# Optimization experiments

Hardware: AMD Instinct MI355X
Metric: run time of the kernel (lower is better)

Reference implementation:

```python
import jax, jax.numpy as jnp
import numpy as np

N = 10000
D1, D2, D3, N_INPUT = 20, 256, 128, 500


def setup_inputs() -> dict:
    key = jax.random.key(0)
    k1, k2, k3, k4, k5 = jax.random.split(key, 5)
    z_igae = jax.random.normal(k1, (N, D1), dtype=jnp.float32)
    # row-stochastic-ish dense (normalized) adjacency stand-in
    adj = jax.random.uniform(k2, (N, N), dtype=jnp.float32) / N
    w3 = jax.random.normal(k3, (D1, D2), dtype=jnp.float32) * 0.1
    w4 = jax.random.normal(k4, (D2, D3), dtype=jnp.float32) * 0.1
    w5 = jax.random.normal(k5, (D3, N_INPUT), dtype=jnp.float32) * 0.1
    return {"z_igae": z_igae, "adj": adj, "w3": w3, "w4": w4, "w5": w5}


def reference(z_igae, adj, w3, w4, w5):
    # GNNLayer: spmm(adj, x @ W), tanh activation when active=True
    z = jnp.tanh(adj @ (z_igae @ w3))        # [N, D2]
    z = jnp.tanh(adj @ (z @ w4))             # [N, D3]
    z_hat = adj @ (z @ w5)                   # [N, n_input], active=False
    z_hat_adj = jax.nn.sigmoid(z_hat @ z_hat.T)  # [N, N] dense reconstruction
    return (z_hat, z_hat_adj)
```

## Files before the change

kernel.cpp:

```cpp
#include <hip/hip_runtime.h>
#include <cstddef>
#include <cstdint>


typedef __attribute__((ext_vector_type(8))) short bf16x8;
typedef __attribute__((ext_vector_type(4))) float f32x4;

#define NROWS 10000
#define MP 10048
#define MP2 10112

__device__ inline unsigned short f2bf(float f) {
  union { float f; unsigned int u; } a; a.f = f;
  unsigned int u = a.u;
  u += 0x7fffu + ((u >> 16) & 1u);
  return (unsigned short)(u >> 16);
}

__device__ inline void gl_lds16(const void* g, void* l) {
  __builtin_amdgcn_global_load_lds(
      (const __attribute__((address_space(1))) void*)g,
      (__attribute__((address_space(3))) void*)l, 16, 0, 0);
}

__global__ __launch_bounds__(256)
void gemm1_fused(const float* __restrict__ adj, const short* __restrict__ zt,
                 short* __restrict__ adjb, float* __restrict__ P,
                 int kChunks, int S) {
  __shared__ short As[64 * 64];
  __shared__ short Bs[32 * 64];
  const int tid  = threadIdx.x;
  const int wave = tid >> 6;
  const int lane = tid & 63;
  const int row0 = blockIdx.y * 64;
  const int s    = blockIdx.z;
  const int t0 = (int)((long long)s * kChunks / S);
  const int t1 = (int)((long long)(s + 1) * kChunks / S);

  f32x4 acc[2];
#pragma unroll
  for (int i = 0; i < 2; ++i) acc[i] = (f32x4){0.f, 0.f, 0.f, 0.f};

  const int lr = lane >> 3;
  const int lk = ((lane & 7) ^ lr) * 8;
  const int fr = lane & 15, fq = lane >> 4, sw = lane & 7;

  const int ar  = tid >> 2;
  const int acq = tid & 3;
  const int gr  = row0 + ar;
  const bool rv = gr < NROWS;

  for (int t = t0; t < t1; ++t) {
    const int k0 = t * 64;
    __syncthreads();
    gl_lds16(zt + (size_t)(8 * wave + lr) * MP + k0 + lk, (void*)(Bs + wave * 512));
    const int gc = k0 + acq * 16;
    float4 f[4];
#pragma unroll
    for (int j = 0; j < 4; ++j) {
      int c = gc + 4 * j;
      f[j] = (rv && c < NROWS) ? *(const float4*)(adj + (size_t)gr * NROWS + c)
                               : make_float4(0.f, 0.f, 0.f, 0.f);
    }
    unsigned short h[16] __attribute__((aligned(16)));
#pragma unroll
    for (int j = 0; j < 4; ++j) {
      h[4 * j + 0] = f2bf(f[j].x); h[4 * j + 1] = f2bf(f[j].y);
      h[4 * j + 2] = f2bf(f[j].z); h[4 * j + 3] = f2bf(f[j].w);
    }
    *(uint4*)(adjb + (size_t)gr * MP + gc)     = *(const uint4*)&h[0];
    *(uint4*)(adjb + (size_t)gr * MP + gc + 8) = *(const uint4*)&h[8];
    *(bf16x8*)&As[ar * 64 + ((acq * 2 + 0) ^ (ar & 7)) * 8] = *(const bf16x8*)&h[0];
    *(bf16x8*)&As[ar * 64 + ((acq * 2 + 1) ^ (ar & 7)) * 8] = *(const bf16x8*)&h[8];
    __syncthreads();
#pragma unroll
    for (int ks = 0; ks < 2; ++ks) {
      const int go = ((ks * 4 + fq) ^ sw) * 8;
      bf16x8 af = *(const bf16x8*)&As[(wave * 16 + fr) * 64 + go];
#pragma unroll
      for (int nt = 0; nt < 2; ++nt) {
        bf16x8 bfr = *(const bf16x8*)&Bs[(nt * 16 + fr) * 64 + go];
        acc[nt] = __builtin_amdgcn_mfma_f32_16x16x32_bf16(af, bfr, acc[nt], 0, 0, 0);
      }
    }
  }
  float* Cs = P + (size_t)s * MP * 32;
  const int rbase = row0 + wave * 16 + (lane >> 4) * 4;
  const int cbase = lane & 15;
#pragma unroll
  for (int nt = 0; nt < 2; ++nt) {
    const int cc = cbase + nt * 16;
#pragma unroll
    for (int r = 0; r < 4; ++r)
      Cs[(size_t)(rbase + r) * 32 + cc] = acc[nt][r];
  }
}

template <int NT>
__global__ __launch_bounds__(256)
void gemm_bf16(const short* __restrict__ A, int lda,
               const short* __restrict__ Bt, int ldb,
               float* __restrict__ C, long long cSplitStride, int ldc,
               int kChunks, int S) {
  __shared__ short As[2][64 * 64];
  __shared__ short Bs[2][NT * 64];
  const int tid  = threadIdx.x;
  const int wave = tid >> 6;
  const int lane = tid & 63;
  const int row0 = blockIdx.y * 64;
  const int col0 = blockIdx.x * NT;
  const int s    = blockIdx.z;
  const int t0 = (int)((long long)s * kChunks / S);
  const int t1 = (int)((long long)(s + 1) * kChunks / S);

  f32x4 acc[NT / 16];
#pragma unroll
  for (int i = 0; i < NT / 16; ++i) acc[i] = (f32x4){0.f, 0.f, 0.f, 0.f};

  const int lr = lane >> 3;
  const int lk = ((lane & 7) ^ lr) * 8;
  const int fr = lane & 15, fq = lane >> 4, sw = lane & 7;

  auto stage = [&](int b, int t) {
    const int k0 = t * 64;
#pragma unroll
    for (int i = 0; i < 2; ++i) {
      int c = wave + 4 * i;
      gl_lds16(A + (size_t)(row0 + 8 * c + lr) * lda + k0 + lk,
               (void*)(&As[b][c * 512]));
    }
#pragma unroll
    for (int i = 0; i < NT / 32; ++i) {
      int c = wave + 4 * i;
      gl_lds16(Bt + (size_t)(col0 + 8 * c + lr) * ldb + k0 + lk,
               (void*)(&Bs[b][c * 512]));
    }
  };

  stage(0, t0);
  for (int t = t0; t < t1; ++t) {
    const int b = (t - t0) & 1;
    __syncthreads();
    if (t + 1 < t1) stage(b ^ 1, t + 1);
#pragma unroll
    for (int ks = 0; ks < 2; ++ks) {
      const int go = ((ks * 4 + fq) ^ sw) * 8;
      bf16x8 af = *(const bf16x8*)&As[b][(wave * 16 + fr) * 64 + go];
#pragma unroll
      for (int nt = 0; nt < NT / 16; ++nt) {
        bf16x8 bfr = *(const bf16x8*)&Bs[b][(nt * 16 + fr) * 64 + go];
        acc[nt] = __builtin_amdgcn_mfma_f32_16x16x32_bf16(af, bfr, acc[nt], 0, 0, 0);
      }
    }
  }

  float* Cs = C + (long long)s * cSplitStride;
  const int rbase = row0 + wave * 16 + (lane >> 4) * 4;
  const int cbase = col0 + (lane & 15);
#pragma unroll
  for (int nt = 0; nt < NT / 16; ++nt) {
    const int cc = cbase + nt * 16;
#pragma unroll
    for (int r = 0; r < 4; ++r)
      Cs[(size_t)(rbase + r) * ldc + cc] = acc[nt][r];
  }
}

__global__ __launch_bounds__(256)
void gemm_recon(const short* __restrict__ A, const short* __restrict__ Bt,
                float* __restrict__ C) {
  __shared__ short As[128 * 64];
  __shared__ short Bs[128 * 64];
  const int tid  = threadIdx.x;
  const int wave = tid >> 6;
  const int lane = tid & 63;
  const int row0 = blockIdx.y * 128;
  const int col0 = blockIdx.x * 128;

  f32x4 acc[2][8];
#pragma unroll
  for (int i = 0; i < 2; ++i)
#pragma unroll
    for (int j = 0; j < 8; ++j) acc[i][j] = (f32x4){0.f, 0.f, 0.f, 0.f};

  const int lr = lane >> 3;
  const int lk = ((lane & 7) ^ lr) * 8;
  const int fr = lane & 15, fq = lane >> 4, sw = lane & 7;

  for (int t = 0; t < 2; ++t) {
    const int k0 = t * 64;
    __syncthreads();
#pragma unroll
    for (int i = 0; i < 4; ++i) {
      int c = wave + 4 * i;
      gl_lds16(A + (size_t)(row0 + 8 * c + lr) * 128 + k0 + lk, (void*)(As + c * 512));
      gl_lds16(Bt + (size_t)(col0 + 8 * c + lr) * 128 + k0 + lk, (void*)(Bs + c * 512));
    }
    __syncthreads();
#pragma unroll
    for (int ks = 0; ks < 2; ++ks) {
      const int go = ((ks * 4 + fq) ^ sw) * 8;
      bf16x8 a0 = *(const bf16x8*)&As[(wave * 32 + fr) * 64 + go];
      bf16x8 a1 = *(const bf16x8*)&As[(wave * 32 + 16 + fr) * 64 + go];
#pragma unroll
      for (int nt = 0; nt < 8; ++nt) {
        bf16x8 bfr = *(const bf16x8*)&Bs[(nt * 16 + fr) * 64 + go];
        acc[0][nt] = __builtin_amdgcn_mfma_f32_16x16x32_bf16(a0, bfr, acc[0][nt], 0, 0, 0);
        acc[1][nt] = __builtin_amdgcn_mfma_f32_16x16x32_bf16(a1, bfr, acc[1][nt], 0, 0, 0);
      }
    }
  }

  const int q = lane >> 4;
#pragma unroll
  for (int mf = 0; mf < 2; ++mf) {
    const int rb = row0 + wave * 32 + mf * 16 + q * 4;
#pragma unroll
    for (int nt = 0; nt < 8; ++nt) {
      const int cc = col0 + nt * 16 + (lane & 15);
      if (cc >= NROWS) continue;
#pragma unroll
      for (int r = 0; r < 4; ++r) {
        const int rr = rb + r;
        if (rr < NROWS) {
          float v = acc[mf][nt][r];
          v = 1.0f / (1.0f + __expf(-v));
          C[(size_t)rr * NROWS + cc] = v;
        }
      }
    }
  }
}

#define TK 16
#define TM 64
#define TN 64

template <int ACT, bool OBF16>
__global__ __launch_bounds__(256)
void gemm_nn_f32(const float* __restrict__ A, int lda,
                 const float* __restrict__ B, int ldb,
                 void* __restrict__ Cp, int ldc, int M, int N, int K) {
  __shared__ float Asm[TK][TM + 4];
  __shared__ float Bsm[TK][TN + 4];
  const int tid = threadIdx.x;
  const int tx = tid & 15, ty = tid >> 4;
  const int row0 = blockIdx.y * TM, col0 = blockIdx.x * TN;
  const int a_m = tid >> 2, a_k = (tid & 3) << 2;
  const int b_k = tid >> 4, b_n = (tid & 15) << 2;
  float acc[4][4] = {};
  const int ntile = (K + TK - 1) / TK;

  auto ld_a = [&](int k0) {
    float4 v = make_float4(0.f, 0.f, 0.f, 0.f);
    int r = row0 + a_m, k = k0 + a_k;
    if (r < M && k < K) v = *(const float4*)(A + (size_t)r * lda + k);
    return v;
  };
  auto ld_b = [&](int k0) {
    float4 v = make_float4(0.f, 0.f, 0.f, 0.f);
    int k = k0 + b_k, c = col0 + b_n;
    if (k < K && c + 3 < N) v = *(const float4*)(B + (size_t)k * ldb + c);
    return v;
  };

  float4 pa = ld_a(0), pb = ld_b(0);
  for (int t = 0; t < ntile; ++t) {
    __syncthreads();
    Asm[a_k + 0][a_m] = pa.x; Asm[a_k + 1][a_m] = pa.y;
    Asm[a_k + 2][a_m] = pa.z; Asm[a_k + 3][a_m] = pa.w;
    *(float4*)&Bsm[b_k][b_n] = pb;
    __syncthreads();
    if (t + 1 < ntile) { pa = ld_a((t + 1) * TK); pb = ld_b((t + 1) * TK); }
#pragma unroll
    for (int kk = 0; kk < TK; ++kk) {
      float4 a = *(const float4*)&Asm[kk][ty << 2];
      float4 b = *(const float4*)&Bsm[kk][tx << 2];
      float av[4] = {a.x, a.y, a.z, a.w};
      float bv[4] = {b.x, b.y, b.z, b.w};
#pragma unroll
      for (int i = 0; i < 4; ++i)
#pragma unroll
        for (int j = 0; j < 4; ++j) acc[i][j] += av[i] * bv[j];
    }
  }
#pragma unroll
  for (int i = 0; i < 4; ++i) {
    int r = row0 + (ty << 2) + i;
    if (r >= M) continue;
#pragma unroll
    for (int j = 0; j < 4; ++j) {
      int c = col0 + (tx << 2) + j;
      if (c >= N) continue;
      float v = acc[i][j];
      if (ACT == 1) v = tanhf(v);
      if (OBF16) ((unsigned short*)Cp)[(size_t)r * ldc + c] = f2bf(v);
      else       ((float*)Cp)[(size_t)r * ldc + c] = v;
    }
  }
}

template <int ACT>
__global__ __launch_bounds__(256)
void gemm_nt_f32(const float* __restrict__ A, int lda,
                 const float* __restrict__ B, int ldb,
                 float* __restrict__ C, int ldc, int M, int N, int K) {
  __shared__ float Asm[TK][TM + 4];
  __shared__ float Bsm[TK][TN + 4];
  const int tid = threadIdx.x;
  const int tx = tid & 15, ty = tid >> 4;
  const int row0 = blockIdx.y * TM, col0 = blockIdx.x * TN;
  const int a_m = tid >> 2, a_k = (tid & 3) << 2;
  const int b_n = tid >> 2, b_k = (tid & 3) << 2;
  float acc[4][4] = {};
  const int ntile = (K + TK - 1) / TK;

  auto ld_a = [&](int k0) {
    float4 v = make_float4(0.f, 0.f, 0.f, 0.f);
    int r = row0 + a_m, k = k0 + a_k;
    if (r < M && k + 3 < K) v = *(const float4*)(A + (size_t)r * lda + k);
    return v;
  };
  auto ld_b = [&](int k0) {
    float4 v = make_float4(0.f, 0.f, 0.f, 0.f);
    int c = col0 + b_n, k = k0 + b_k;
    if (c < N && k + 3 < K) v = *(const float4*)(B + (size_t)c * ldb + k);
    return v;
  };

  float4 pa = ld_a(0), pb = ld_b(0);
  for (int t = 0; t < ntile; ++t) {
    __syncthreads();
    Asm[a_k + 0][a_m] = pa.x; Asm[a_k + 1][a_m] = pa.y;
    Asm[a_k + 2][a_m] = pa.z; Asm[a_k + 3][a_m] = pa.w;
    Bsm[b_k + 0][b_n] = pb.x; Bsm[b_k + 1][b_n] = pb.y;
    Bsm[b_k + 2][b_n] = pb.z; Bsm[b_k + 3][b_n] = pb.w;
    __syncthreads();
    if (t + 1 < ntile) { pa = ld_a((t + 1) * TK); pb = ld_b((t + 1) * TK); }
#pragma unroll
    for (int kk = 0; kk < TK; ++kk) {
      float4 a = *(const float4*)&Asm[kk][ty << 2];
      float4 b = *(const float4*)&Bsm[kk][tx << 2];
      float av[4] = {a.x, a.y, a.z, a.w};
      float bv[4] = {b.x, b.y, b.z, b.w};
#pragma unroll
      for (int i = 0; i < 4; ++i)
#pragma unroll
        for (int j = 0; j < 4; ++j) acc[i][j] += av[i] * bv[j];
    }
  }
#pragma unroll
  for (int i = 0; i < 4; ++i) {
    int r = row0 + (ty << 2) + i;
    if (r >= M) continue;
#pragma unroll
    for (int j = 0; j < 4; ++j) {
      int c = col0 + (tx << 2) + j;
      if (c >= N) continue;
      C[(size_t)r * ldc + c] = acc[i][j];
    }
  }
}


__global__ void tr_zigae(const float* __restrict__ z, short* __restrict__ zt) {
  int m = blockIdx.x * 256 + threadIdx.x;
  int n = blockIdx.y;
  if (m >= MP) return;
  float v = (n < 20 && m < NROWS) ? z[(size_t)m * 20 + n] : 0.f;
  zt[(size_t)n * MP + m] = f2bf(v);
}

__global__ void transpose_c128(const float* __restrict__ in, int M,
                               short* __restrict__ out) {
  __shared__ float tile[32][33];
  int m0 = blockIdx.x * 32, n0 = blockIdx.y * 32;
  int tx = threadIdx.x, ty = threadIdx.y;
  for (int i = ty; i < 32; i += 8) {
    int m = m0 + i;
    tile[i][tx] = (m < M) ? in[(size_t)m * 128 + n0 + tx] : 0.f;
  }
  __syncthreads();
  for (int i = ty; i < 32; i += 8) {
    int n = n0 + i, m = m0 + tx;
    if (m < MP) out[(size_t)n * MP + m] = f2bf(tile[tx][i]);
  }
}

__global__ void reduce_g1(const float* __restrict__ P, float* __restrict__ g1) {
  int m = blockIdx.x * 4 + (threadIdx.x >> 5);
  int n = threadIdx.x & 31;
  if (m >= NROWS) return;
  float s = 0.f;
#pragma unroll
  for (int i = 0; i < 8; ++i) s += P[(size_t)i * MP * 32 + (size_t)m * 32 + n];
  g1[(size_t)m * 32 + n] = s;
}

__global__ __launch_bounds__(256)
void reduce_tr(const float* __restrict__ P, short* __restrict__ z2t) {
  __shared__ float T[128][33];
  const int tid = threadIdx.x;
  const int m0 = blockIdx.x * 32;
  const int mr = tid >> 5;
  const int n0 = (tid & 31) * 4;
#pragma unroll
  for (int g = 0; g < 4; ++g) {
    const int mm = g * 8 + mr;
    const int m = m0 + mm;
    f32x4 sAcc = (f32x4){0.f, 0.f, 0.f, 0.f};
#pragma unroll
    for (int i = 0; i < 8; ++i) {
      f32x4 v = *(const f32x4*)(P + (size_t)i * MP * 128 + (size_t)m * 128 + n0);
      sAcc += v;
    }
    if (m < NROWS) {
      T[n0 + 0][mm] = tanhf(sAcc[0]); T[n0 + 1][mm] = tanhf(sAcc[1]);
      T[n0 + 2][mm] = tanhf(sAcc[2]); T[n0 + 3][mm] = tanhf(sAcc[3]);
    } else {
      T[n0 + 0][mm] = 0.f; T[n0 + 1][mm] = 0.f;
      T[n0 + 2][mm] = 0.f; T[n0 + 3][mm] = 0.f;
    }
  }
  __syncthreads();
  const int n = tid >> 1, mh = (tid & 1) * 16;
  unsigned short h[16] __attribute__((aligned(16)));
#pragma unroll
  for (int j = 0; j < 16; ++j) h[j] = f2bf(T[n][mh + j]);
  *(uint4*)(z2t + (size_t)n * MP + m0 + mh)     = *(const uint4*)&h[0];
  *(uint4*)(z2t + (size_t)n * MP + m0 + mh + 8) = *(const uint4*)&h[8];
}

template <int ACT>
__global__ void reduce128(const float* __restrict__ P, float* __restrict__ outf,
                          short* __restrict__ outb, int M) {
  int m = blockIdx.x, n = threadIdx.x;
  if (m >= M) { if (outb) outb[(size_t)m * 128 + n] = 0; return; }
  float s = 0.f;
#pragma unroll
  for (int i = 0; i < 8; ++i) s += P[(size_t)i * MP * 128 + (size_t)m * 128 + n];
  if (ACT == 1) s = tanhf(s);
  if (outf) outf[(size_t)m * 128 + n] = s;
  if (outb) outb[(size_t)m * 128 + n] = f2bf(s);
}

__global__ void zero_bf16(short* p, int n) {
  int i = blockIdx.x * 256 + threadIdx.x;
  if (i < n) p[i] = 0;
}

extern "C" void kernel_launch(void* const* d_in, const int* in_sizes, int n_in,
                              void* d_out, int out_size, void* d_ws, size_t ws_size,
                              hipStream_t stream) {
  const float* z_igae = (const float*)d_in[0];
  const float* adj    = (const float*)d_in[1];
  const float* w3     = (const float*)d_in[2];
  const float* w4     = (const float*)d_in[3];
  const float* w5     = (const float*)d_in[4];

  const int M = NROWS, D2 = 256, D3 = 128, NI = 500;
  const int S = 8, KC = MP / 64;

  float* z_hat   = (float*)d_out;
  float* out_adj = (float*)d_out + (size_t)M * NI;

  char* oa = (char*)out_adj;
  short* adjb = (short*)oa;
  float* P    = (float*)(oa + 204ll * 1024 * 1024);
  char*  sc   = oa + 248ll * 1024 * 1024;
  float* z1   = (float*)(sc);
  float* t2   = (float*)(sc + 11ll * 1024 * 1024);
  short* t2t  = (short*)(sc + 17ll * 1024 * 1024);
  short* z2t  = (short*)(sc + 20ll * 1024 * 1024);
  float* g1   = (float*)(sc + 23ll * 1024 * 1024);
  short* zt   = (short*)(sc + 25ll * 1024 * 1024);
  float* Mm   = (float*)(sc + 26ll * 1024 * 1024);
  float* g3   = (float*)(sc + 27ll * 1024 * 1024);

  short* hb  = (short*)d_ws;
  short* g3b = (short*)d_ws + (size_t)MP2 * 128;

  dim3 blk(256);
  const int MT = 157;

  tr_zigae<<<dim3(40, 32), blk, 0, stream>>>(z_igae, zt);
  gemm1_fused<<<dim3(1, MT, S), blk, 0, stream>>>(adj, zt, adjb, P, KC, S);
  reduce_g1<<<dim3(2500), dim3(128), 0, stream>>>(P, g1);
  gemm_nn_f32<1, false><<<dim3(4, MT), blk, 0, stream>>>(g1, 32, w3, D2, z1, D2, M, D2, 20);
  gemm_nn_f32<0, false><<<dim3(2, MT), blk, 0, stream>>>(z1, D2, w4, D3, t2, D3, M, D3, D2);
  transpose_c128<<<dim3(314, 4), dim3(32, 8), 0, stream>>>(t2, M, t2t);
  gemm_bf16<128><<<dim3(1, MT, S), blk, 0, stream>>>(
      adjb, MP, t2t, MP, P, (long long)MP * 128, 128, KC, S);
  reduce_tr<<<dim3(314), blk, 0, stream>>>(P, z2t);
  gemm_bf16<128><<<dim3(1, MT, S), blk, 0, stream>>>(
      adjb, MP, z2t, MP, P, (long long)MP * 128, 128, KC, S);
  reduce128<0><<<dim3(MP2), dim3(128), 0, stream>>>(P, g3, g3b, M);
  gemm_nn_f32<0, false><<<dim3(8, MT), blk, 0, stream>>>(g3, D3, w5, NI, z_hat, NI, M, NI, D3);
  gemm_nt_f32<0><<<dim3(2, 2), blk, 0, stream>>>(w5, NI, w5, NI, Mm, D3, D3, D3, NI);
  gemm_nn_f32<0, true><<<dim3(2, MT), blk, 0, stream>>>(g3, D3, Mm, D3, (void*)hb, D3, M, D3, D3);
  zero_bf16<<<dim3(56), blk, 0, stream>>>(hb + (size_t)M * 128, (MP2 - M) * 128);
  gemm_recon<<<dim3(79, 79), blk, 0, stream>>>(hb, g3b, out_adj);
}
```

Before: 1.023 ms.

## Fuse mid-chain dense ops and enlarge adjacency GEMM tiles to 128 rows

Replaces the 64-row double-buffered adjacency GEMM with a 128x128-tile kernel in which each wave computes a 64x64 block. The kernel is single-buffered and synchronised twice per k-step, so each A tile is reused across more output columns. Merges the g1 reduction, the w3 multiply with tanh, the w4 multiply and the transpose into one midchain kernel. Also merges the g3 reduction with the Mm projection into hb, which drops several launches and intermediate round-trips to global memory. In exchange, the adjacency GEMM loses its load/compute overlap, and the bigger register and LDS footprint may reduce occupancy, since only 79x8 blocks are launched.

After: 1.084 ms. 5.9% more time.

```diff
diff --git a/kernel.cpp b/kernel.cpp
--- a/kernel.cpp
+++ b/kernel.cpp
@@ -7,8 +7,8 @@
 typedef __attribute__((ext_vector_type(4))) float f32x4;
 
 #define NROWS 10000
-#define MP 10048
-#define MP2 10112
+#define MP    10048
+#define MPAD  10112
 
 __device__ inline unsigned short f2bf(float f) {
   union { float f; unsigned int u; } a; a.f = f;
@@ -84,7 +84,7 @@
       }
     }
   }
-  float* Cs = P + (size_t)s * MP * 32;
+  float* Cs = P + (size_t)s * MPAD * 32;
   const int rbase = row0 + wave * 16 + (lane >> 4) * 4;
   const int cbase = lane & 15;
 #pragma unroll
@@ -96,73 +96,70 @@
   }
 }
 
-template <int NT>
-__global__ __launch_bounds__(256)
-void gemm_bf16(const short* __restrict__ A, int lda,
-               const short* __restrict__ Bt, int ldb,
-               float* __restrict__ C, long long cSplitStride, int ldc,
-               int kChunks, int S) {
-  __shared__ short As[2][64 * 64];
-  __shared__ short Bs[2][NT * 64];
+__global__ __launch_bounds__(256)
+void gemm_adj(const short* __restrict__ A, const short* __restrict__ Bt,
+              float* __restrict__ P, int kChunks, int S) {
+  __shared__ short As[128 * 64];
+  __shared__ short Bs[128 * 64];
   const int tid  = threadIdx.x;
   const int wave = tid >> 6;
   const int lane = tid & 63;
-  const int row0 = blockIdx.y * 64;
-  const int col0 = blockIdx.x * NT;
+  const int row0 = blockIdx.y * 128;
   const int s    = blockIdx.z;
   const int t0 = (int)((long long)s * kChunks / S);
   const int t1 = (int)((long long)(s + 1) * kChunks / S);
-
-  f32x4 acc[NT / 16];
-#pragma unroll
-  for (int i = 0; i < NT / 16; ++i) acc[i] = (f32x4){0.f, 0.f, 0.f, 0.f};
+  const int wr = wave >> 1, wc = wave & 1;
+
+  f32x4 acc[4][4];
+#pragma unroll
+  for (int m = 0; m < 4; ++m)
+#pragma unroll
+    for (int n = 0; n < 4; ++n) acc[m][n] = (f32x4){0.f, 0.f, 0.f, 0.f};
 
   const int lr = lane >> 3;
   const int lk = ((lane & 7) ^ lr) * 8;
   const int fr = lane & 15, fq = lane >> 4, sw = lane & 7;
 
-  auto stage = [&](int b, int t) {
+  for (int t = t0; t < t1; ++t) {
     const int k0 = t * 64;
-#pragma unroll
-    for (int i = 0; i < 2; ++i) {
+    __syncthreads();
+#pragma unroll
+    for (int i = 0; i < 4; ++i) {
       int c = wave + 4 * i;
-      gl_lds16(A + (size_t)(row0 + 8 * c + lr) * lda + k0 + lk,
-               (void*)(&As[b][c * 512]));
-    }
-#pragma unroll
-    for (int i = 0; i < NT / 32; ++i) {
-      int c = wave + 4 * i;
-      gl_lds16(Bt + (size_t)(col0 + 8 * c + lr) * ldb + k0 + lk,
-               (void*)(&Bs[b][c * 512]));
-    }
-  };
-
-  stage(0, t0);
-  for (int t = t0; t < t1; ++t) {
-    const int b = (t - t0) & 1;
-    __syncthreads();
-    if (t + 1 < t1) stage(b ^ 1, t + 1);
+      gl_lds16(A + (size_t)(row0 + 8 * c + lr) * MP + k0 + lk, (void*)(As + c * 512));
+      gl_lds16(Bt + (size_t)(8 * c + lr) * MP + k0 + lk, (void*)(Bs + c * 512));
+    }
+    __syncthreads();
 #pragma unroll
     for (int ks = 0; ks < 2; ++ks) {
       const int go = ((ks * 4 + fq) ^ sw) * 8;
-      bf16x8 af = *(const bf16x8*)&As[b][(wave * 16 + fr) * 64 + go];
-#pragma unroll
-      for (int nt = 0; nt < NT / 16; ++nt) {
-        bf16x8 bfr = *(const bf16x8*)&Bs[b][(nt * 16 + fr) * 64 + go];
-        acc[nt] = __builtin_amdgcn_mfma_f32_16x16x32_bf16(af, bfr, acc[nt], 0, 0, 0);
-      }
-    }
-  }
-
-  float* Cs = C + (long long)s * cSplitStride;
-  const int rbase = row0 + wave * 16 + (lane >> 4) * 4;
-  const int cbase = col0 + (lane & 15);
-#pragma unroll
-  for (int nt = 0; nt < NT / 16; ++nt) {
-    const int cc = cbase + nt * 16;
-#pragma unroll
-    for (int r = 0; r < 4; ++r)
-      Cs[(size_t)(rbase + r) * ldc + cc] = acc[nt][r];
+      bf16x8 av[4], bv[4];
+#pragma unroll
+      for (int m = 0; m < 4; ++m)
+        av[m] = *(const bf16x8*)&As[(wr * 64 + m * 16 + fr) * 64 + go];
+#pragma unroll
+      for (int n = 0; n < 4; ++n)
+        bv[n] = *(const bf16x8*)&Bs[(wc * 64 + n * 16 + fr) * 64 + go];
+#pragma unroll
+      for (int m = 0; m < 4; ++m)
+#pragma unroll
+        for (int n = 0; n < 4; ++n)
+          acc[m][n] = __builtin_amdgcn_mfma_f32_16x16x32_bf16(av[m], bv[n], acc[m][n], 0, 0, 0);
+    }
+  }
+
+  float* Cs = P + (size_t)s * MPAD * 128;
+  const int q = lane >> 4;
+#pragma unroll
+  for (int m = 0; m < 4; ++m) {
+    const int rb = row0 + wr * 64 + m * 16 + q * 4;
+#pragma unroll
+    for (int n = 0; n < 4; ++n) {
+      const int cc = wc * 64 + n * 16 + fr;
+#pragma unroll
+      for (int r = 0; r < 4; ++r)
+        Cs[(size_t)(rb + r) * 128 + cc] = acc[m][n][r];
+    }
   }
 }
 
@@ -232,15 +229,138 @@
   }
 }
 
+__global__ __launch_bounds__(256)
+void midchain(const float* __restrict__ P, const float* __restrict__ w3,
+              const float* __restrict__ w4, short* __restrict__ t2t) {
+  __shared__ float w3s[20][256];
+  __shared__ float g1s[64][36];
+  __shared__ float z1s[64][260];
+  __shared__ float bufB[64][132];
+  const int tid = threadIdx.x;
+  const int m0  = blockIdx.x * 64;
+
+  for (int j = tid; j < 20 * 256; j += 256) w3s[j >> 8][j & 255] = w3[j];
+  {
+    const int r = tid >> 2, c0 = (tid & 3) * 8;
+    f32x4 s0 = {0.f, 0.f, 0.f, 0.f}, s1 = {0.f, 0.f, 0.f, 0.f};
+#pragma unroll
+    for (int i = 0; i < 8; ++i) {
+      const float* p = P + (size_t)i * MPAD * 32 + (size_t)(m0 + r) * 32 + c0;
+      s0 += *(const f32x4*)p;
+      s1 += *(const f32x4*)(p + 4);
+    }
+    *(f32x4*)&g1s[r][c0] = s0;
+    *(f32x4*)&g1s[r][c0 + 4] = s1;
+  }
+  __syncthreads();
+  {
+    const int r = tid >> 2, c0 = (tid & 3) * 64;
+    float a[20];
+#pragma unroll
+    for (int k = 0; k < 20; ++k) a[k] = g1s[r][k];
+    for (int c = 0; c < 64; c += 4) {
+      f32x4 s = {0.f, 0.f, 0.f, 0.f};
+#pragma unroll
+      for (int k = 0; k < 20; ++k) s += a[k] * *(const f32x4*)&w3s[k][c0 + c];
+      z1s[r][c0 + c + 0] = tanhf(s[0]); z1s[r][c0 + c + 1] = tanhf(s[1]);
+      z1s[r][c0 + c + 2] = tanhf(s[2]); z1s[r][c0 + c + 3] = tanhf(s[3]);
+    }
+  }
+  const int r = tid >> 2, c0 = (tid & 3) * 32;
+  float acc[32];
+#pragma unroll
+  for (int j = 0; j < 32; ++j) acc[j] = 0.f;
+  for (int kt = 0; kt < 4; ++kt) {
+    __syncthreads();
+    {
+      const int lr = tid >> 2, lc = (tid & 3) * 32;
+#pragma unroll
+      for (int j = 0; j < 32; j += 4)
+        *(f32x4*)&bufB[lr][lc + j] =
+            *(const f32x4*)(w4 + (size_t)(kt * 64 + lr) * 128 + lc + j);
+    }
+    __syncthreads();
+    for (int k = 0; k < 64; ++k) {
+      const float a = z1s[r][kt * 64 + k];
+#pragma unroll
+      for (int j = 0; j < 32; j += 4) {
+        f32x4 w = *(const f32x4*)&bufB[k][c0 + j];
+        acc[j + 0] += a * w[0]; acc[j + 1] += a * w[1];
+        acc[j + 2] += a * w[2]; acc[j + 3] += a * w[3];
+      }
+    }
+  }
+  __syncthreads();
+#pragma unroll
+  for (int j = 0; j < 32; j += 4) *(f32x4*)&bufB[r][c0 + j] = *(const f32x4*)&acc[j];
+  __syncthreads();
+  {
+    const int n = tid >> 1, seg = (tid & 1) * 32;
+    unsigned short h[32] __attribute__((aligned(16)));
+#pragma unroll
+    for (int i = 0; i < 32; ++i) h[i] = f2bf(bufB[seg + i][n]);
+    uint4* dst = (uint4*)(t2t + (size_t)n * MP + m0 + seg);
+    dst[0] = *(const uint4*)&h[0];  dst[1] = *(const uint4*)&h[8];
+    dst[2] = *(const uint4*)&h[16]; dst[3] = *(const uint4*)&h[24];
+  }
+}
+
+__global__ __launch_bounds__(256)
+void reduce128h(const float* __restrict__ P, const float* __restrict__ Mm,
+                float* __restrict__ g3, short* __restrict__ g3b,
+                short* __restrict__ hb) {
+  __shared__ float MmS[128 * 128];
+  __shared__ float g3t[64][132];
+  const int tid = threadIdx.x;
+  const int m0  = blockIdx.x * 64;
+
+  for (int j = tid; j < 128 * 128; j += 256) MmS[j] = Mm[j];
+  const int r = tid >> 2, c0 = (tid & 3) * 32;
+  {
+    const int gr = m0 + r;
+    for (int c = 0; c < 32; c += 4) {
+      f32x4 s = {0.f, 0.f, 0.f, 0.f};
+#pragma unroll
+      for (int i = 0; i < 8; ++i)
+        s += *(const f32x4*)(P + (size_t)i * MPAD * 128 + (size_t)gr * 128 + c0 + c);
+      *(f32x4*)&g3t[r][c0 + c] = s;
+      *(f32x4*)(g3 + (size_t)gr * 128 + c0 + c) = s;
+      short4 sb;
+      sb.x = (short)f2bf(s[0]); sb.y = (short)f2bf(s[1]);
+      sb.z = (short)f2bf(s[2]); sb.w = (short)f2bf(s[3]);
+      *(short4*)(g3b + (size_t)gr * 128 + c0 + c) = sb;
+    }
+  }
+  __syncthreads();
+  float acc[32];
+#pragma unroll
+  for (int j = 0; j < 32; ++j) acc[j] = 0.f;
+  for (int k = 0; k < 128; ++k) {
+    const float a = g3t[r][k];
+#pragma unroll
+    for (int j = 0; j < 32; j += 4) {
+      const float* mv = &MmS[k * 128 + c0 + j];
+      acc[j + 0] += a * mv[0]; acc[j + 1] += a * mv[1];
+      acc[j + 2] += a * mv[2]; acc[j + 3] += a * mv[3];
+    }
+  }
+  unsigned short h[32] __attribute__((aligned(16)));
+#pragma unroll
+  for (int j = 0; j < 32; ++j) h[j] = f2bf(acc[j]);
+  uint4* dst = (uint4*)(hb + (size_t)(m0 + r) * 128 + c0);
+  dst[0] = *(const uint4*)&h[0]; dst[1] = *(const uint4*)&h[8];
+  dst[2] = *(const uint4*)&h[16]; dst[3] = *(const uint4*)&h[24];
+}
+
 #define TK 16
 #define TM 64
 #define TN 64
 
-template <int ACT, bool OBF16>
+template <int ACT>
 __global__ __launch_bounds__(256)
 void gemm_nn_f32(const float* __restrict__ A, int lda,
                  const float* __restrict__ B, int ldb,
-                 void* __restrict__ Cp, int ldc, int M, int N, int K) {
+                 float* __restrict__ C, int ldc, int M, int N, int K) {
   __shared__ float Asm[TK][TM + 4];
   __shared__ float Bsm[TK][TN + 4];
   const int tid = threadIdx.x;
@@ -294,13 +414,11 @@
       if (c >= N) continue;
       float v = acc[i][j];
       if (ACT == 1) v = tanhf(v);
-      if (OBF16) ((unsigned short*)Cp)[(size_t)r * ldc + c] = f2bf(v);
-      else       ((float*)Cp)[(size_t)r * ldc + c] = v;
-    }
-  }
-}
-
-template <int ACT>
+      C[(size_t)r * ldc + c] = v;
+    }
+  }
+}
+
 __global__ __launch_bounds__(256)
 void gemm_nt_f32(const float* __restrict__ A, int lda,
                  const float* __restrict__ B, int ldb,
@@ -371,32 +489,6 @@
   zt[(size_t)n * MP + m] = f2bf(v);
 }
 
-__global__ void transpose_c128(const float* __restrict__ in, int M,
-                               short* __restrict__ out) {
-  __shared__ float tile[32][33];
-  int m0 = blockIdx.x * 32, n0 = blockIdx.y * 32;
-  int tx = threadIdx.x, ty = threadIdx.y;
-  for (int i = ty; i < 32; i += 8) {
-    int m = m0 + i;
-    tile[i][tx] = (m < M) ? in[(size_t)m * 128 + n0 + tx] : 0.f;
-  }
-  __syncthreads();
-  for (int i = ty; i < 32; i += 8) {
-    int n = n0 + i, m = m0 + tx;
-    if (m < MP) out[(size_t)n * MP + m] = f2bf(tile[tx][i]);
-  }
-}
-
-__global__ void reduce_g1(const float* __restrict__ P, float* __restrict__ g1) {
-  int m = blockIdx.x * 4 + (threadIdx.x >> 5);
-  int n = threadIdx.x & 31;
-  if (m >= NROWS) return;
-  float s = 0.f;
-#pragma unroll
-  for (int i = 0; i < 8; ++i) s += P[(size_t)i * MP * 32 + (size_t)m * 32 + n];
-  g1[(size_t)m * 32 + n] = s;
-}
-
 __global__ __launch_bounds__(256)
 void reduce_tr(const float* __restrict__ P, short* __restrict__ z2t) {
   __shared__ float T[128][33];
@@ -410,10 +502,8 @@
     const int m = m0 + mm;
     f32x4 sAcc = (f32x4){0.f, 0.f, 0.f, 0.f};
 #pragma unroll
-    for (int i = 0; i < 8; ++i) {
-      f32x4 v = *(const f32x4*)(P + (size_t)i * MP * 128 + (size_t)m * 128 + n0);
-      sAcc += v;
-    }
+    for (int i = 0; i < 8; ++i)
+      sAcc += *(const f32x4*)(P + (size_t)i * MPAD * 128 + (size_t)m * 128 + n0);
     if (m < NROWS) {
       T[n0 + 0][mm] = tanhf(sAcc[0]); T[n0 + 1][mm] = tanhf(sAcc[1]);
       T[n0 + 2][mm] = tanhf(sAcc[2]); T[n0 + 3][mm] = tanhf(sAcc[3]);
@@ -429,24 +519,6 @@
   for (int j = 0; j < 16; ++j) h[j] = f2bf(T[n][mh + j]);
   *(uint4*)(z2t + (size_t)n * MP + m0 + mh)     = *(const uint4*)&h[0];
   *(uint4*)(z2t + (size_t)n * MP + m0 + mh + 8) = *(const uint4*)&h[8];
-}
-
-template <int ACT>
-__global__ void reduce128(const float* __restrict__ P, float* __restrict__ outf,
-                          short* __restrict__ outb, int M) {
-  int m = blockIdx.x, n = threadIdx.x;
-  if (m >= M) { if (outb) outb[(size_t)m * 128 + n] = 0; return; }
-  float s = 0.f;
-#pragma unroll
-  for (int i = 0; i < 8; ++i) s += P[(size_t)i * MP * 128 + (size_t)m * 128 + n];
-  if (ACT == 1) s = tanhf(s);
-  if (outf) outf[(size_t)m * 128 + n] = s;
-  if (outb) outb[(size_t)m * 128 + n] = f2bf(s);
-}
-
-__global__ void zero_bf16(short* p, int n) {
-  int i = blockIdx.x * 256 + threadIdx.x;
-  if (i < n) p[i] = 0;
 }
 
 extern "C" void kernel_launch(void* const* d_in, const int* in_sizes, int n_in,
@@ -468,36 +540,25 @@
   short* adjb = (short*)oa;
   float* P    = (float*)(oa + 204ll * 1024 * 1024);
   char*  sc   = oa + 248ll * 1024 * 1024;
-  float* z1   = (float*)(sc);
-  float* t2   = (float*)(sc + 11ll * 1024 * 1024);
-  short* t2t  = (short*)(sc + 17ll * 1024 * 1024);
-  short* z2t  = (short*)(sc + 20ll * 1024 * 1024);
-  float* g1   = (float*)(sc + 23ll * 1024 * 1024);
-  short* zt   = (short*)(sc + 25ll * 1024 * 1024);
-  float* Mm   = (float*)(sc + 26ll * 1024 * 1024);
-  float* g3   = (float*)(sc + 27ll * 1024 * 1024);
+  short* t2t  = (short*)(sc);
+  short* z2t  = (short*)(sc + 3ll * 1024 * 1024);
+  short* zt   = (short*)(sc + 6ll * 1024 * 1024);
+  float* Mm   = (float*)(sc + 7ll * 1024 * 1024);
+  float* g3   = (float*)(sc + 8ll * 1024 * 1024);
 
   short* hb  = (short*)d_ws;
-  short* g3b = (short*)d_ws + (size_t)MP2 * 128;
+  short* g3b = (short*)d_ws + (size_t)MPAD * 128;
 
   dim3 blk(256);
-  const int MT = 157;
-
+
+  gemm_nt_f32<<<dim3(2, 2), blk, 0, stream>>>(w5, NI, w5, NI, Mm, D3, D3, D3, NI);
   tr_zigae<<<dim3(40, 32), blk, 0, stream>>>(z_igae, zt);
-  gemm1_fused<<<dim3(1, MT, S), blk, 0, stream>>>(adj, zt, adjb, P, KC, S);
-  reduce_g1<<<dim3(2500), dim3(128), 0, stream>>>(P, g1);
-  gemm_nn_f32<1, false><<<dim3(4, MT), blk, 0, stream>>>(g1, 32, w3, D2, z1, D2, M, D2, 20);
-  gemm_nn_f32<0, false><<<dim3(2, MT), blk, 0, stream>>>(z1, D2, w4, D3, t2, D3, M, D3, D2);
-  transpose_c128<<<dim3(314, 4), dim3(32, 8), 0, stream>>>(t2, M, t2t);
-  gemm_bf16<128><<<dim3(1, MT, S), blk, 0, stream>>>(
-      adjb, MP, t2t, MP, P, (long long)MP * 128, 128, KC, S);
+  gemm1_fused<<<dim3(1, 158, S), blk, 0, stream>>>(adj, zt, adjb, P, KC, S);
+  midchain<<<dim3(157), blk, 0, stream>>>(P, w3, w4, t2t);
+  gemm_adj<<<dim3(1, 79, S), blk, 0, stream>>>(adjb, t2t, P, KC, S);
   reduce_tr<<<dim3(314), blk, 0, stream>>>(P, z2t);
-  gemm_bf16<128><<<dim3(1, MT, S), blk, 0, stream>>>(
-      adjb, MP, z2t, MP, P, (long long)MP * 128, 128, KC, S);
-  reduce128<0><<<dim3(MP2), dim3(128), 0, stream>>>(P, g3, g3b, M);
-  gemm_nn_f32<0, false><<<dim3(8, MT), blk, 0, stream>>>(g3, D3, w5, NI, z_hat, NI, M, NI, D3);
-  gemm_nt_f32<0><<<dim3(2, 2), blk, 0, stream>>>(w5, NI, w5, NI, Mm, D3, D3, D3, NI);
-  gemm_nn_f32<0, true><<<dim3(2, MT), blk, 0, stream>>>(g3, D3, Mm, D3, (void*)hb, D3, M, D3, D3);
-  zero_bf16<<<dim3(56), blk, 0, stream>>>(hb + (size_t)M * 128, (MP2 - M) * 128);
+  gemm_adj<<<dim3(1, 79, S), blk, 0, stream>>>(adjb, z2t, P, KC, S);
+  reduce128h<<<dim3(158), blk, 0, stream>>>(P, Mm, g3, g3b, hb);
+  gemm_nn_f32<0><<<dim3(8, 157), blk, 0, stream>>>(g3, D3, w5, NI, z_hat, NI, M, NI, D3);
   gemm_recon<<<dim3(79, 79), blk, 0, stream>>>(hb, g3b, out_adj);
 }
```
